# Performance work log

Measured on AMD Instinct MI355X. Metric: run time of the kernel, lower is better.

Reference implementation:

```python
import jax, jax.numpy as jnp
import numpy as np

N_HEAD = 8

def setup_inputs() -> dict:
    key = jax.random.key(0)
    ks = jax.random.split(key, 5)
    B, T, C = 2, 4096, 512
    x = jax.random.normal(ks[0], (B, T, C), dtype=jnp.float32)
    w_attn = jax.random.normal(ks[1], (3 * C, C), dtype=jnp.float32) * (1.0 / np.sqrt(C))
    b_attn = jax.random.normal(ks[2], (3 * C,), dtype=jnp.float32) * 0.02
    w_proj = jax.random.normal(ks[3], (C, C), dtype=jnp.float32) * (1.0 / np.sqrt(C))
    b_proj = jax.random.normal(ks[4], (C,), dtype=jnp.float32) * 0.02
    return {"x": x, "w_attn": w_attn, "b_attn": b_attn, "w_proj": w_proj, "b_proj": b_proj}

def reference(x, w_attn, b_attn, w_proj, b_proj):
    B, T, C = x.shape
    H = N_HEAD
    D = C // H  # head dim
    qkv = x @ w_attn.T + b_attn  # [B,T,3C]
    q, k, v = jnp.split(qkv, 3, axis=-1)
    # b t (h d) -> b h t d
    def to_heads(t):
        return t.reshape(B, T, H, D).transpose(0, 2, 1, 3)
    q, k, v = to_heads(q), to_heads(k), to_heads(v)
    scale = 1.0 / np.sqrt(D).astype(np.float32)
    att = jnp.einsum('bhqd,bhkd->bhqk', q, k) * scale  # [B,H,T,T]
    causal = jnp.tril(jnp.ones((T, T), dtype=bool))
    att = jnp.where(causal[None, None], att, jnp.float32(-jnp.inf))
    att = jax.nn.softmax(att, axis=-1)
    y = jnp.einsum('bhqk,bhkd->bhqd', att, v)  # [B,H,T,D]
    y = y.transpose(0, 2, 1, 3).reshape(B, T, C)
    return y @ w_proj.T + b_proj
```

## Files before the change

### kernel.cpp

```cpp
#include <hip/hip_runtime.h>

typedef __attribute__((ext_vector_type(8))) __bf16 bf16x8;
typedef __attribute__((ext_vector_type(4))) __bf16 bf16x4;
typedef __attribute__((ext_vector_type(4))) float f32x4;
typedef __attribute__((ext_vector_type(16))) float f32x16;
typedef __attribute__((ext_vector_type(4))) unsigned uint32x4;
typedef __attribute__((ext_vector_type(2))) unsigned uint32x2;

#define AS1 __attribute__((address_space(1)))
#define AS3 __attribute__((address_space(3)))

#if __has_builtin(__builtin_amdgcn_exp2f)
#define EXP2(x) __builtin_amdgcn_exp2f(x)
#else
#define EXP2(x) exp2f(x)
#endif

#define QSCALE 0.18033688011112042f

#define N_X 4194304
#define N_WA 786432
#define N_WP 262144
__global__ __launch_bounds__(256) void convert_all_k(const float* __restrict__ x,
                                                     const float* __restrict__ wa,
                                                     const float* __restrict__ wp,
                                                     __bf16* __restrict__ xb,
                                                     __bf16* __restrict__ wab,
                                                     __bf16* __restrict__ wpb) {
  int i = (blockIdx.x * 256 + threadIdx.x) * 4;
  const float* src;
  __bf16* dst;
  int off;
  if (i < N_X)              { src = x;  dst = xb;  off = i; }
  else if (i < N_X + N_WA)  { src = wa; dst = wab; off = i - N_X; }
  else if (i < N_X + N_WA + N_WP) { src = wp; dst = wpb; off = i - N_X - N_WA; }
  else return;
  float4 v = *reinterpret_cast<const float4*>(src + off);
  bf16x4 o;
  o[0] = (__bf16)v.x; o[1] = (__bf16)v.y; o[2] = (__bf16)v.z; o[3] = (__bf16)v.w;
  *reinterpret_cast<bf16x4*>(dst + off) = o;
}

template <int EPI>
__global__ __launch_bounds__(256) void gemm_bt(const __bf16* __restrict__ A,
                                               const __bf16* __restrict__ Bm,
                                               const float* __restrict__ bias,
                                               void* __restrict__ outp,
                                               __bf16* __restrict__ vtout,
                                               int M, int N, int K) {
  __shared__ __bf16 smem[16384];
  __bf16* a_lds = smem;
  __bf16* b_lds = smem + 8192;
  const int tid = threadIdx.x;
  const int lane = tid & 63;
  const int w = tid >> 6;
  const int wm = w >> 1, wn = w & 1;
  const int ll = lane & 15, lh = lane >> 4;
  const int bid = (int)blockIdx.x;
  const int NT = N >> 7;
  const int xcd = bid & 7, lidx = bid >> 3;
  const int m0 = (xcd * 8 + lidx / NT) * 128;
  const int n0 = (lidx % NT) * 128;
  f32x4 acc[4][4] = {};

  for (int k0 = 0; k0 < K; k0 += 64) {
    __syncthreads();
#pragma unroll
    for (int i = 0; i < 4; ++i) {
      int ch = i * 256 + w * 64 + lane;
      int r = ch >> 3, c8 = (ch & 7) ^ (r & 7);
      const __bf16* ga = A + (size_t)(m0 + r) * K + k0 + c8 * 8;
      __builtin_amdgcn_global_load_lds((const AS1 void*)ga,
                                       (AS3 void*)(a_lds + (i * 256 + w * 64) * 8), 16, 0, 0);
      const __bf16* gb = Bm + (size_t)(n0 + r) * K + k0 + c8 * 8;
      __builtin_amdgcn_global_load_lds((const AS1 void*)gb,
                                       (AS3 void*)(b_lds + (i * 256 + w * 64) * 8), 16, 0, 0);
    }
    __syncthreads();
#pragma unroll
    for (int kc = 0; kc < 2; ++kc) {
      bf16x8 af[4], bfr[4];
#pragma unroll
      for (int m = 0; m < 4; ++m) {
        int R = wm * 64 + m * 16 + ll;
        af[m] = *reinterpret_cast<const bf16x8*>(a_lds + R * 64 + (((kc * 4 + lh) ^ (R & 7)) << 3));
      }
#pragma unroll
      for (int n = 0; n < 4; ++n) {
        int R = wn * 64 + n * 16 + ll;
        bfr[n] = *reinterpret_cast<const bf16x8*>(b_lds + R * 64 + (((kc * 4 + lh) ^ (R & 7)) << 3));
      }
#pragma unroll
      for (int m = 0; m < 4; ++m)
#pragma unroll
        for (int n = 0; n < 4; ++n)
          acc[m][n] = __builtin_amdgcn_mfma_f32_16x16x32_bf16(af[m], bfr[n], acc[m][n], 0, 0, 0);
    }
  }
  if (EPI == 1) {
#pragma unroll
    for (int m = 0; m < 4; ++m) {
      int gm = m0 + wm * 64 + m * 16 + lh * 4;
#pragma unroll
      for (int n = 0; n < 4; ++n) {
        int gn = n0 + wn * 64 + n * 16 + ll;
        float bs = bias[gn];
#pragma unroll
        for (int r = 0; r < 4; ++r)
          ((float*)outp)[(size_t)(gm + r) * N + gn] = acc[m][n][r] + bs;
      }
    }
  } else if (n0 < 1024) {
    __syncthreads();
    __bf16* tb = smem + w * 4096;
    const float sc = (n0 < 512) ? (float)QSCALE : 1.0f;
#pragma unroll
    for (int m = 0; m < 4; ++m)
#pragma unroll
      for (int n = 0; n < 4; ++n) {
        float bs = bias[n0 + wn * 64 + n * 16 + ll];
#pragma unroll
        for (int r = 0; r < 4; ++r)
          tb[(m * 16 + lh * 4 + r) * 64 + n * 16 + ll] = (__bf16)((acc[m][n][r] + bs) * sc);
      }
    const int rsub = lane >> 3, csub = (lane & 7) * 8;
#pragma unroll
    for (int i = 0; i < 8; ++i) {
      bf16x8 vv = *reinterpret_cast<const bf16x8*>(tb + (i * 8 + rsub) * 64 + csub);
      *reinterpret_cast<bf16x8*>((__bf16*)outp +
          (size_t)(m0 + wm * 64 + i * 8 + rsub) * N + n0 + wn * 64 + csub) = vv;
    }
  } else {
    __syncthreads();
    __bf16* tb = smem + w * 4096;
#pragma unroll
    for (int m = 0; m < 4; ++m) {
      const int rb = m * 4 + lh;
#pragma unroll
      for (int n = 0; n < 4; ++n) {
        const int col = n * 16 + ll;
        float bs = bias[n0 + wn * 64 + col];
        bf16x4 pk;
#pragma unroll
        for (int r = 0; r < 4; ++r) pk[r] = (__bf16)(acc[m][n][r] + bs);
        *reinterpret_cast<bf16x4*>(tb + col * 64 + ((rb ^ (col & 15)) << 2)) = pk;
      }
    }
    const int b = m0 >> 12;
    const int tbase = (m0 + wm * 64) & 4095;
    const int dbase = n0 - 1024 + wn * 64;
    const int dl = lane >> 3;
    const int j1 = (lane & 7) * 2;
    const int tloc = (lane & 7) * 8;
#pragma unroll
    for (int i = 0; i < 8; ++i) {
      const int col = i * 8 + dl;
      uint32x2 lo = *reinterpret_cast<const uint32x2*>(tb + col * 64 + ((j1 ^ (col & 15)) << 2));
      uint32x2 hi = *reinterpret_cast<const uint32x2*>(tb + col * 64 + (((j1 + 1) ^ (col & 15)) << 2));
      uint32x4 full = {lo[0], lo[1], hi[0], hi[1]};
      *reinterpret_cast<uint32x4*>(vtout + ((size_t)(b * 512 + dbase + col)) * 4096 + tbase + tloc) = full;
    }
  }
}

struct Tbl { unsigned short t[204]; };
constexpr Tbl build_tbl() {
  Tbl T{};
  int sizes[204] = {};
  int n = 0;
  for (int p = 0; p < 2; ++p)
    for (int qx = 0; qx < 32; ++qx) {
      int total = 2 * qx + 2;
      int nch = (total + 11) / 12;
      int cum = 0;
      for (int q = 0; q < qx; ++q) cum += (2 * q + 13) / 12;
      for (int c = 0; c < nch; ++c) {
        int sz = total - 12 * c; if (sz > 12) sz = 12;
        T.t[n] = (unsigned short)(qx | (c << 5) | (p << 8) | ((cum + c) << 9));
        sizes[n] = sz;
        ++n;
      }
    }
  for (int i = 1; i < n; ++i) {
    unsigned short tv = T.t[i]; int sv = sizes[i];
    int j = i - 1;
    while (j >= 0 && sizes[j] < sv) { T.t[j + 1] = T.t[j]; sizes[j + 1] = sizes[j]; --j; }
    T.t[j + 1] = tv; sizes[j + 1] = sv;
  }
  return T;
}
__device__ __constant__ Tbl g_tbl = build_tbl();

__device__ inline unsigned cvtpk(float lo, float hi_) {
  unsigned r;
  asm("v_cvt_pk_bf16_f32 %0, %1, %2" : "=v"(r) : "v"(lo), "v"(hi_));
  return r;
}

__global__ __launch_bounds__(256, 4) void attn_k(const __bf16* __restrict__ qkv,
                                                 const __bf16* __restrict__ vt,
                                                 __bf16* __restrict__ opart,
                                                 float* __restrict__ lpart,
                                                 __bf16* __restrict__ y) {
  __shared__ __bf16 k_lds[3][64 * 64];
  __shared__ __bf16 v_lds[2][64 * 64];
  const int tid = threadIdx.x, lane = tid & 63, w = tid >> 6;
  const int hi = lane >> 5, q31 = lane & 31;
  const int swz = q31 & 7;

  const int bid = (int)blockIdx.x;
  const int e = g_tbl.t[bid >> 3];
  const int qx = e & 31, c = (e >> 5) & 7, p = (e >> 8) & 1, j = e >> 9;
  const int bh = (bid & 7) * 2 + p;
  const int pslot = bh * 102 + j;
  const int b = bh >> 3, h = bh & 7;
  const int q0 = qx * 128;
  const int qw0 = q0 + w * 32;
  const int t0 = 12 * c;
  const int t1 = min(12 * c + 12, 2 * qx + 2);

  const __bf16* qp = qkv + (size_t)b * 4096 * 1536 + h * 64;
  const __bf16* vtp = vt + (size_t)(b * 512 + h * 64) * 4096;

  const int rr = tid >> 3;
  const int cs = (tid & 7) ^ (rr & 7);
  const __bf16* kg = qp + 512 + (size_t)(t0 * 64 + rr) * 1536 + cs * 8;
  const __bf16* vg = vtp + (size_t)rr * 4096 + t0 * 64 + cs * 8;

  bf16x8 qf[4];
  {
    const __bf16* qr = qp + (size_t)(qw0 + q31) * 1536 + hi * 8;
#pragma unroll
    for (int d = 0; d < 4; ++d) qf[d] = *reinterpret_cast<const bf16x8*>(qr + d * 16);
  }

  f32x16 o0 = {}, o1 = {};
  float l_run = 0.f;

  auto stageK = [&](int ks) {
    __builtin_amdgcn_global_load_lds((const AS1 void*)kg,
        (AS3 void*)(&k_lds[ks][w * 512]), 16, 0, 0);
    __builtin_amdgcn_global_load_lds((const AS1 void*)(kg + 32 * 1536),
        (AS3 void*)(&k_lds[ks][2048 + w * 512]), 16, 0, 0);
    kg += 64 * 1536;
  };
  auto stageV = [&](int vs) {
    __builtin_amdgcn_global_load_lds((const AS1 void*)vg,
        (AS3 void*)(&v_lds[vs][w * 512]), 16, 0, 0);
    __builtin_amdgcn_global_load_lds((const AS1 void*)(vg + 32 * 4096),
        (AS3 void*)(&v_lds[vs][2048 + w * 512]), 16, 0, 0);
    vg += 64;
  };

  stageV(0);
  __builtin_amdgcn_sched_barrier(0);
  stageK(0);
  __builtin_amdgcn_sched_barrier(0);
  stageK(1);
  __builtin_amdgcn_sched_barrier(0);

  int kslot = 0, vslot = 0;
  for (int t = t0; t < t1; ++t) {
    if (t + 1 < t1) asm volatile("s_waitcnt vmcnt(2)" ::: "memory");
    else            asm volatile("s_waitcnt vmcnt(0)" ::: "memory");
    __builtin_amdgcn_sched_barrier(0);
    __builtin_amdgcn_s_barrier();
    __builtin_amdgcn_sched_barrier(0);
    if (t + 1 < t1) {
      stageV(vslot ^ 1);
      __builtin_amdgcn_sched_barrier(0);
      if (t + 2 < t1) {
        int k2 = kslot + 2; if (k2 >= 3) k2 -= 3;
        stageK(k2);
        __builtin_amdgcn_sched_barrier(0);
      }
    }
    const int kv0 = t * 64;
    if (kv0 <= qw0 + 31) {
      f32x16 s0 = {}, s1 = {};
      __builtin_amdgcn_s_setprio(1);
#pragma unroll
      for (int d = 0; d < 4; ++d) {
        int c0 = ((d * 2 + hi) ^ swz) * 8;
        s0 = __builtin_amdgcn_mfma_f32_32x32x16_bf16(
            *reinterpret_cast<const bf16x8*>(&k_lds[kslot][q31 * 64 + c0]), qf[d], s0, 0, 0, 0);
        s1 = __builtin_amdgcn_mfma_f32_32x32x16_bf16(
            *reinterpret_cast<const bf16x8*>(&k_lds[kslot][(32 + q31) * 64 + c0]), qf[d], s1, 0, 0, 0);
      }
      __builtin_amdgcn_s_setprio(0);
      if (kv0 + 63 > qw0) {
        const int q = qw0 + q31;
#pragma unroll
        for (int r = 0; r < 16; ++r) {
          int crow = (r & 3) + 8 * (r >> 2) + 4 * hi;
          if (kv0 + crow > q) s0[r] = -1e30f;
          if (kv0 + 32 + crow > q) s1[r] = -1e30f;
        }
      }
#pragma unroll
      for (int r = 0; r < 16; ++r) s0[r] = EXP2(s0[r]);
#pragma unroll
      for (int r = 0; r < 16; ++r) s1[r] = EXP2(s1[r]);
      {
        float a8[8];
#pragma unroll
        for (int r = 0; r < 8; ++r)
          a8[r] = (s0[r] + s0[r + 8]) + (s1[r] + s1[r + 8]);
        l_run += (((a8[0] + a8[1]) + (a8[2] + a8[3])) + ((a8[4] + a8[5]) + (a8[6] + a8[7])));
      }
      uint32x4 pa[4];
#pragma unroll
      for (int half = 0; half < 2; ++half) {
        const int bse = half * 8;
        {
          unsigned x1 = cvtpk(s0[bse + 0], s0[bse + 1]);
          unsigned y1 = cvtpk(s0[bse + 4], s0[bse + 5]);
          asm("v_permlane32_swap_b32 %0, %1" : "+v"(x1), "+v"(y1));
          pa[half][0] = x1; pa[half][2] = y1;
          unsigned x2 = cvtpk(s0[bse + 2], s0[bse + 3]);
          unsigned y2 = cvtpk(s0[bse + 6], s0[bse + 7]);
          asm("v_permlane32_swap_b32 %0, %1" : "+v"(x2), "+v"(y2));
          pa[half][1] = x2; pa[half][3] = y2;
        }
        {
          unsigned x1 = cvtpk(s1[bse + 0], s1[bse + 1]);
          unsigned y1 = cvtpk(s1[bse + 4], s1[bse + 5]);
          asm("v_permlane32_swap_b32 %0, %1" : "+v"(x1), "+v"(y1));
          pa[2 + half][0] = x1; pa[2 + half][2] = y1;
          unsigned x2 = cvtpk(s1[bse + 2], s1[bse + 3]);
          unsigned y2 = cvtpk(s1[bse + 6], s1[bse + 7]);
          asm("v_permlane32_swap_b32 %0, %1" : "+v"(x2), "+v"(y2));
          pa[2 + half][1] = x2; pa[2 + half][3] = y2;
        }
      }
      __builtin_amdgcn_s_setprio(1);
#pragma unroll
      for (int ks = 0; ks < 4; ++ks) {
        int c0 = ((ks * 2 + hi) ^ swz) * 8;
        bf16x8 pfrag = __builtin_bit_cast(bf16x8, pa[ks]);
        o0 = __builtin_amdgcn_mfma_f32_32x32x16_bf16(
            *reinterpret_cast<const bf16x8*>(&v_lds[vslot][q31 * 64 + c0]), pfrag, o0, 0, 0, 0);
        o1 = __builtin_amdgcn_mfma_f32_32x32x16_bf16(
            *reinterpret_cast<const bf16x8*>(&v_lds[vslot][(32 + q31) * 64 + c0]), pfrag, o1, 0, 0, 0);
      }
      __builtin_amdgcn_s_setprio(0);
    }
    __builtin_amdgcn_sched_barrier(0);
    kslot = (kslot == 2) ? 0 : kslot + 1;
    vslot ^= 1;
  }

  l_run += __shfl_xor(l_run, 32);

  const int rloc = w * 32 + q31;
  if (t0 == 0 && t1 == 2 * qx + 2) {
    const float inv = 1.f / l_run;
    __bf16* yr = y + ((size_t)b * 4096 + qw0 + q31) * 512 + h * 64;
#pragma unroll
    for (int g = 0; g < 4; ++g) {
      bf16x4 v0, v1;
#pragma unroll
      for (int jj = 0; jj < 4; ++jj) {
        v0[jj] = (__bf16)(o0[g * 4 + jj] * inv);
        v1[jj] = (__bf16)(o1[g * 4 + jj] * inv);
      }
      *reinterpret_cast<bf16x4*>(yr + 8 * g + 4 * hi) = v0;
      *reinterpret_cast<bf16x4*>(yr + 32 + 8 * g + 4 * hi) = v1;
    }
  } else {
    __bf16* ob = opart + ((size_t)pslot * 128 + rloc) * 64;
#pragma unroll
    for (int g = 0; g < 4; ++g) {
      bf16x4 v0, v1;
#pragma unroll
      for (int jj = 0; jj < 4; ++jj) {
        v0[jj] = (__bf16)(o0[g * 4 + jj]);
        v1[jj] = (__bf16)(o1[g * 4 + jj]);
      }
      *reinterpret_cast<bf16x4*>(ob + 8 * g + 4 * hi) = v0;
      *reinterpret_cast<bf16x4*>(ob + 32 + 8 * g + 4 * hi) = v1;
    }
    if (hi == 0) lpart[pslot * 128 + rloc] = l_run;
  }
}

__global__ __launch_bounds__(256) void combine_k(const __bf16* __restrict__ opart,
                                                 const float* __restrict__ lpart,
                                                 __bf16* __restrict__ y) {
  const int bid = (int)blockIdx.x;
  const int bh = bid >> 5, qx = bid & 31;
  if (qx < 6) return;
  const int b = bh >> 3, h = bh & 7;
  const int n = (2 * qx + 13) / 12;
  int cum = 0;
  for (int q = 0; q < qx; ++q) cum += (2 * q + 13) / 12;
  const int g0 = bh * 102 + cum;
  const int tid = threadIdx.x;
  const int r = tid >> 1, dh = (tid & 1) * 32;

  float W = 0.f;
  float acc[32] = {};
  for (int i = 0; i < n; ++i) {
    W += lpart[(g0 + i) * 128 + r];
    const __bf16* op = opart + ((size_t)(g0 + i) * 128 + r) * 64 + dh;
#pragma unroll
    for (int jj = 0; jj < 4; ++jj) {
      bf16x8 v = *reinterpret_cast<const bf16x8*>(op + jj * 8);
#pragma unroll
      for (int e = 0; e < 8; ++e) acc[jj * 8 + e] += (float)v[e];
    }
  }
  const float inv = 1.f / W;
  __bf16* yr = y + ((size_t)b * 4096 + qx * 128 + r) * 512 + h * 64 + dh;
#pragma unroll
  for (int jj = 0; jj < 4; ++jj) {
    bf16x8 ov;
#pragma unroll
    for (int e = 0; e < 8; ++e) ov[e] = (__bf16)(acc[jj * 8 + e] * inv);
    *reinterpret_cast<bf16x8*>(yr + jj * 8) = ov;
  }
}

extern "C" void kernel_launch(void* const* d_in, const int* in_sizes, int n_in,
                              void* d_out, int out_size, void* d_ws, size_t ws_size,
                              hipStream_t stream) {
  const float* x      = (const float*)d_in[0];
  const float* w_attn = (const float*)d_in[1];
  const float* b_attn = (const float*)d_in[2];
  const float* w_proj = (const float*)d_in[3];
  const float* b_proj = (const float*)d_in[4];
  float* out = (float*)d_out;

  const int Bv = 2, T = 4096, C = 512;
  const int M = Bv * T;

  const size_t NPART = (size_t)1632 * 128 * 64;
  __bf16* opart  = (__bf16*)d_ws;
  __bf16* x_bf   = opart;
  __bf16* wa_bf  = opart + NPART;
  __bf16* wp_bf  = wa_bf + (size_t)786432;
  __bf16* qkv_bf = wp_bf + (size_t)262144;
  __bf16* y_bf   = qkv_bf + (size_t)12582912;
  __bf16* vt_bf  = y_bf + (size_t)4194304;
  float*  lpart  = (float*)(vt_bf + (size_t)4194304);

  const int ntot = N_X + N_WA + N_WP;
  convert_all_k<<<(ntot / 4 + 255) / 256, 256, 0, stream>>>(x, w_attn, w_proj, x_bf, wa_bf, wp_bf);

  gemm_bt<0><<<dim3((3 * C / 128) * (M / 128)), 256, 0, stream>>>(x_bf, wa_bf, b_attn, qkv_bf, vt_bf, M, 3 * C, C);
  attn_k<<<dim3(1632), 256, 0, stream>>>(qkv_bf, vt_bf, opart, lpart, y_bf);
  combine_k<<<dim3(512), 256, 0, stream>>>(opart, lpart, y_bf);
  gemm_bt<1><<<dim3((C / 128) * (M / 128)), 256, 0, stream>>>(y_bf, wp_bf, b_proj, out, nullptr, M, C, C);
}
```

Measured before the change: 106.4 us.

## Double-buffer GEMM K-loop with 32-wide stages and XCD-aware combine mapping

Restructures the GEMM main loop from a single-buffered BK=64 tile with two barriers per step into a double-buffered BK=32 pipeline. The next stage is prefetched via global_load_lds while the current stage feeds MFMAs, with one barrier per step and raised wave priority around the MFMA block. It also remaps combine_k block indices so that each XCD handles contiguous batch-head groups. The costs are twice as many loop iterations with smaller tiles and a full vmcnt(0) wait each step, which limits how much load and compute actually overlap.

New measurement: 102.6 us. 1.04x faster.

```diff
diff --git a/kernel.cpp b/kernel.cpp
--- a/kernel.cpp
+++ b/kernel.cpp
@@ -49,8 +49,6 @@
                                                __bf16* __restrict__ vtout,
                                                int M, int N, int K) {
   __shared__ __bf16 smem[16384];
-  __bf16* a_lds = smem;
-  __bf16* b_lds = smem + 8192;
   const int tid = threadIdx.x;
   const int lane = tid & 63;
   const int w = tid >> 6;
@@ -63,39 +61,52 @@
   const int n0 = (lidx % NT) * 128;
   f32x4 acc[4][4] = {};
 
-  for (int k0 = 0; k0 < K; k0 += 64) {
-    __syncthreads();
-#pragma unroll
-    for (int i = 0; i < 4; ++i) {
-      int ch = i * 256 + w * 64 + lane;
-      int r = ch >> 3, c8 = (ch & 7) ^ (r & 7);
-      const __bf16* ga = A + (size_t)(m0 + r) * K + k0 + c8 * 8;
-      __builtin_amdgcn_global_load_lds((const AS1 void*)ga,
-                                       (AS3 void*)(a_lds + (i * 256 + w * 64) * 8), 16, 0, 0);
-      const __bf16* gb = Bm + (size_t)(n0 + r) * K + k0 + c8 * 8;
-      __builtin_amdgcn_global_load_lds((const AS1 void*)gb,
-                                       (AS3 void*)(b_lds + (i * 256 + w * 64) * 8), 16, 0, 0);
-    }
-    __syncthreads();
-#pragma unroll
-    for (int kc = 0; kc < 2; ++kc) {
-      bf16x8 af[4], bfr[4];
-#pragma unroll
-      for (int m = 0; m < 4; ++m) {
-        int R = wm * 64 + m * 16 + ll;
-        af[m] = *reinterpret_cast<const bf16x8*>(a_lds + R * 64 + (((kc * 4 + lh) ^ (R & 7)) << 3));
-      }
-#pragma unroll
-      for (int n = 0; n < 4; ++n) {
-        int R = wn * 64 + n * 16 + ll;
-        bfr[n] = *reinterpret_cast<const bf16x8*>(b_lds + R * 64 + (((kc * 4 + lh) ^ (R & 7)) << 3));
-      }
-#pragma unroll
-      for (int m = 0; m < 4; ++m)
-#pragma unroll
-        for (int n = 0; n < 4; ++n)
-          acc[m][n] = __builtin_amdgcn_mfma_f32_16x16x32_bf16(af[m], bfr[n], acc[m][n], 0, 0, 0);
-    }
+  auto stage = [&](int k0, int ss) {
+    __bf16* al = smem + ss * 8192;
+    __bf16* bl = al + 4096;
+#pragma unroll
+    for (int i = 0; i < 2; ++i) {
+      int ch = i * 256 + tid;
+      int r = ch >> 2, cs = (ch & 3) ^ (r & 3);
+      const __bf16* ga = A + (size_t)(m0 + r) * K + k0 + cs * 8;
+      __builtin_amdgcn_global_load_lds((const AS1 void*)ga, (AS3 void*)(al + ch * 8), 16, 0, 0);
+      const __bf16* gb = Bm + (size_t)(n0 + r) * K + k0 + cs * 8;
+      __builtin_amdgcn_global_load_lds((const AS1 void*)gb, (AS3 void*)(bl + ch * 8), 16, 0, 0);
+    }
+  };
+
+  stage(0, 0);
+  __builtin_amdgcn_sched_barrier(0);
+  const int nsteps = K >> 5;
+  for (int t = 0; t < nsteps; ++t) {
+    asm volatile("s_waitcnt vmcnt(0)" ::: "memory");
+    __builtin_amdgcn_sched_barrier(0);
+    __builtin_amdgcn_s_barrier();
+    __builtin_amdgcn_sched_barrier(0);
+    if (t + 1 < nsteps) {
+      stage((t + 1) << 5, (t + 1) & 1);
+      __builtin_amdgcn_sched_barrier(0);
+    }
+    const __bf16* al = smem + (t & 1) * 8192;
+    const __bf16* bl = al + 4096;
+    bf16x8 af[4], bfr[4];
+#pragma unroll
+    for (int m = 0; m < 4; ++m) {
+      int R = wm * 64 + m * 16 + ll;
+      af[m] = *reinterpret_cast<const bf16x8*>(al + R * 32 + ((lh ^ (R & 3)) << 3));
+    }
+#pragma unroll
+    for (int n = 0; n < 4; ++n) {
+      int R = wn * 64 + n * 16 + ll;
+      bfr[n] = *reinterpret_cast<const bf16x8*>(bl + R * 32 + ((lh ^ (R & 3)) << 3));
+    }
+    __builtin_amdgcn_s_setprio(1);
+#pragma unroll
+    for (int m = 0; m < 4; ++m)
+#pragma unroll
+      for (int n = 0; n < 4; ++n)
+        acc[m][n] = __builtin_amdgcn_mfma_f32_16x16x32_bf16(af[m], bfr[n], acc[m][n], 0, 0, 0);
+    __builtin_amdgcn_s_setprio(0);
   }
   if (EPI == 1) {
 #pragma unroll
@@ -113,6 +124,7 @@
   } else if (n0 < 1024) {
     __syncthreads();
     __bf16* tb = smem + w * 4096;
+    const int lh4 = lane >> 4;
     const float sc = (n0 < 512) ? (float)QSCALE : 1.0f;
 #pragma unroll
     for (int m = 0; m < 4; ++m)
@@ -121,7 +133,7 @@
         float bs = bias[n0 + wn * 64 + n * 16 + ll];
 #pragma unroll
         for (int r = 0; r < 4; ++r)
-          tb[(m * 16 + lh * 4 + r) * 64 + n * 16 + ll] = (__bf16)((acc[m][n][r] + bs) * sc);
+          tb[(m * 16 + lh4 * 4 + r) * 64 + n * 16 + ll] = (__bf16)((acc[m][n][r] + bs) * sc);
       }
     const int rsub = lane >> 3, csub = (lane & 7) * 8;
 #pragma unroll
@@ -388,7 +400,9 @@
                                                  const float* __restrict__ lpart,
                                                  __bf16* __restrict__ y) {
   const int bid = (int)blockIdx.x;
-  const int bh = bid >> 5, qx = bid & 31;
+  const int xcd = bid & 7, idx = bid >> 3;
+  const int bh = xcd * 2 + (idx >> 5);
+  const int qx = idx & 31;
   if (qx < 6) return;
   const int b = bh >> 3, h = bh & 7;
   const int n = (2 * qx + 13) / 12;
```
